# Kernel tuning notes

Hardware: AMD Instinct MI355X
Metric: run time of the kernel (lower is better)

The kernel has to match this reference:

```python
import jax, jax.numpy as jnp
import numpy as np

B, C, H, W = 8, 256, 64, 64
NUM_LABELS = 16  # labels in {-1, 0..15}; -1 means 'no group'


def setup_inputs() -> dict:
    key = jax.random.key(0)
    kx, kl, kw, kb = jax.random.split(key, 4)
    x = jax.random.normal(kx, (B, C, H, W), dtype=jnp.float32)
    # labels in [-1, NUM_LABELS)
    labels = jax.random.randint(kl, (B * C,), 0, NUM_LABELS + 1) - 1
    # groups=C, kernel 1x1: conv weight is (3C,1,1,1) -> per-output-channel scale; bias (3C,)
    w = jax.random.normal(kw, (3 * C,), dtype=jnp.float32) * 0.5
    b = jax.random.normal(kb, (3 * C,), dtype=jnp.float32) * 0.02
    return {"x": x, "labels": labels, "w": w, "b": b}


def reference(x, labels, w, b):
    # x: (B,C,h,w); labels: (B*C,); w,b: (3C,)
    Bv, Cv, hv, wv = x.shape
    hw = hv * wv
    xf = x.reshape(Bv, Cv, hw)
    # grouped 1x1 conv: out channel o (of 3C) reads input channel o//3
    x_rep = jnp.repeat(xf, 3, axis=1)                      # (B,3C,hw)
    qkv = x_rep * w[None, :, None] + b[None, :, None]      # (B,3C,hw)
    flat = qkv.reshape(Bv * 3 * Cv, hw)                    # matches torch reshape(1,3BC,hw)
    BC = Bv * Cv
    q, k, v = flat[:BC], flat[BC:2 * BC], flat[2 * BC:]    # each (BC, hw)
    valid = labels != -1                                   # (BC,)
    same = (labels[:, None] == labels[None, :]) & valid[:, None] & valid[None, :]
    # per-label-group attention == masked dense attention (softmax over same-label cols only)
    scores = q @ k.T                                       # (BC, BC), no sqrt(d) scaling (as in source)
    neg = jnp.finfo(scores.dtype).min
    scores = jnp.where(same, scores, neg)
    weights = jax.nn.softmax(scores, axis=-1)
    out = weights @ v                                      # (BC, hw)
    out = jnp.where(valid[:, None], out, jnp.zeros((), out.dtype))  # -1 rows stay zero
    return out[None]                                       # (1, BC, hw)
```

## Files before the change

### kernel.cpp

```cpp
#include <hip/hip_runtime.h>
#include <cfloat>

#define B_   8
#define C_   256
#define HW_  4096
#define BC_  2048
#define TC_  768
#define NG_  16
#define MAXG 320
#define UK0  682
#define NUQ  683
#define NUK  684
#define NXU  1366
#define NXALL 2048
#define VLO  1280

#define SPLITK 8
#define NT     11
#define NTILES (NT * NT)
#define KSL    (HW_ / SPLITK)
#define WKC    (KSL / 4)
#define NP1    (NUQ * NUK)
#define QMAX   32639

#define MCAP  192
#define CST   192
#define BKP   216

typedef __attribute__((ext_vector_type(8))) short short8;
typedef __attribute__((ext_vector_type(4))) float floatx4;
typedef __attribute__((ext_vector_type(4))) int   intx4;

__device__ __forceinline__ unsigned short f32_to_bf16_rne(float f) {
  unsigned u = __float_as_uint(f);
  unsigned r = (u + 0x7FFFu + ((u >> 16) & 1u)) >> 16;
  return (unsigned short)r;
}

__global__ __launch_bounds__(256) void prep_kernel(
    const float* __restrict__ x, const int* __restrict__ labels,
    char* __restrict__ q8h, char* __restrict__ q8l,
    unsigned short* __restrict__ xhi, float* __restrict__ sums,
    float* __restrict__ scA, float* __restrict__ scB,
    int* __restrict__ grp_n, int* __restrict__ members,
    int* __restrict__ posArr, int nhi)
{
  const int t = threadIdx.x;
  if (blockIdx.x < NG_) {
    __shared__ int lab[BC_];
    __shared__ int cnts[256];
    const int g = blockIdx.x;
    for (int idx = t; idx < BC_; idx += 256) lab[idx] = labels[idx];
    __syncthreads();
    const int base = t * 8;
    int cnt = 0;
#pragma unroll
    for (int k = 0; k < 8; k++) cnt += (lab[base + k] == g) ? 1 : 0;
    cnts[t] = cnt;
    for (int off = 1; off < 256; off <<= 1) {
      __syncthreads();
      const int v = (t >= off) ? cnts[t - off] : 0;
      __syncthreads();
      cnts[t] += v;
    }
    __syncthreads();
    int pos = cnts[t] - cnt;
    if (t == 255) grp_n[g] = cnts[255] < MAXG ? cnts[255] : MAXG;
#pragma unroll
    for (int k = 0; k < 8; k++) {
      const int i = base + k;
      if (lab[i] == g) {
        if (pos < MAXG) { members[g * MAXG + pos] = i; posArr[i] = pos; }
        pos++;
      }
    }
    return;
  }

  const int u = blockIdx.x - NG_;
  if (u >= nhi) return;
  const float* row = x + (size_t)u * HW_;

  if (u < NXU) {
    __shared__ float xs[HW_];
    __shared__ float red[4];
    float s = 0.f, mx = 0.f;
#pragma unroll
    for (int i = 0; i < 4; i++) {
      const int col = i * 1024 + t * 4;
      const float4 v = *(const float4*)(row + col);
      *(float4*)(xs + col) = v;
      s += v.x + v.y + v.z + v.w;
      mx = fmaxf(mx, fmaxf(fmaxf(fabsf(v.x), fabsf(v.y)),
                           fmaxf(fabsf(v.z), fabsf(v.w))));
    }
#pragma unroll
    for (int o = 32; o > 0; o >>= 1) s += __shfl_down(s, o);
    if ((t & 63) == 0) red[t >> 6] = s;
    __syncthreads();
    const float rowsum = red[0] + red[1] + red[2] + red[3];
    __syncthreads();
#pragma unroll
    for (int o = 32; o > 0; o >>= 1) mx = fmaxf(mx, __shfl_down(mx, o));
    if ((t & 63) == 0) red[t >> 6] = mx;
    __syncthreads();
    const float bmax = fmaxf(fmaxf(fmaxf(red[0], red[1]),
                                   fmaxf(red[2], red[3])), 1e-20f);
    if (t == 0) {
      sums[u] = rowsum;
      const float sc = bmax / (float)QMAX;
      if (u < NUQ)  scA[u] = sc;
      if (u >= UK0) scB[u - UK0] = sc;
    }
    const float sinv = (float)QMAX / bmax;
    char* hrow = q8h + (size_t)u * HW_;
    char* lrow = q8l + (size_t)u * HW_;
#pragma unroll
    for (int i = 0; i < 4; i++) {
      const int col = i * 1024 + t * 4;
      char4 hc, lc;
#pragma unroll
      for (int j = 0; j < 4; j++) {
        int q = __float2int_rn(xs[col + j] * sinv);
        q = q > QMAX ? QMAX : (q < -QMAX ? -QMAX : q);
        const int h = (q + 128) >> 8;
        ((char*)&hc)[j] = (char)h;
        ((char*)&lc)[j] = (char)(q - (h << 8));
      }
      *(char4*)(hrow + col) = hc;
      *(char4*)(lrow + col) = lc;
    }
    if (xhi && u >= VLO) {
      unsigned short* hb = xhi + (size_t)u * HW_;
#pragma unroll
      for (int i = 0; i < 4; i++) {
        const int col = i * 1024 + t * 4;
        ushort4 h;
        h.x = f32_to_bf16_rne(xs[col + 0]);
        h.y = f32_to_bf16_rne(xs[col + 1]);
        h.z = f32_to_bf16_rne(xs[col + 2]);
        h.w = f32_to_bf16_rne(xs[col + 3]);
        *(ushort4*)(hb + col) = h;
      }
    }
  } else {
    unsigned short* hb = xhi + (size_t)u * HW_;
#pragma unroll
    for (int i = 0; i < 4; i++) {
      const int col = i * 1024 + t * 4;
      const float4 v = *(const float4*)(row + col);
      ushort4 h;
      h.x = f32_to_bf16_rne(v.x);
      h.y = f32_to_bf16_rne(v.y);
      h.z = f32_to_bf16_rne(v.z);
      h.w = f32_to_bf16_rne(v.w);
      *(ushort4*)(hb + col) = h;
    }
  }
}

__global__ __launch_bounds__(256) void gram_mfma_kernel(
    const char* __restrict__ q8h, const char* __restrict__ q8l,
    float* __restrict__ P,
    const float* __restrict__ w, const float* __restrict__ bbias,
    const float* __restrict__ sums, const int* __restrict__ grp_n,
    const int* __restrict__ members, float4* __restrict__ gtA,
    float2* __restrict__ gtB)
{
  const int bid  = blockIdx.x;
  const int z    = bid & 7;
  const int tile = bid >> 3;
  const int m0 = (tile % NT) * 64;
  const int n0 = (tile / NT) * 64;

  const int t = threadIdx.x;
  const int wave = t >> 6;
  const int lane = t & 63;
  const int fr = lane & 15;
  const int fq = lane >> 4;

  if (z == 0 && tile < NG_) {
    const int g = tile;
    const int n = grp_n[g];
    for (int p = t; p < n; p += 256) {
      const int j = members[g * MAXG + p];
      const int rk = j + BC_;
      const int jk = rk % TC_;
      const int uk = (rk / TC_) * C_ + jk / 3;
      const int jv = (j + 2 * BC_) % TC_;
      gtA[g * MAXG + p] = make_float4(w[jk], bbias[jk], sums[uk], w[jv]);
      gtB[g * MAXG + p] = make_float2(bbias[jv], __int_as_float(uk - UK0));
    }
  }

  const int kbase = z * KSL + wave * WKC + fq * 16;
  const char *pah[4], *pal[4], *pbh[4], *pbl[4];
#pragma unroll
  for (int i = 0; i < 4; i++) {
    const int ar = min(m0 + fr + i * 16, NUQ - 1);
    const int br = min(UK0 + n0 + fr + i * 16, NXU - 1);
    pah[i] = q8h + (size_t)ar * HW_ + kbase;
    pal[i] = q8l + (size_t)ar * HW_ + kbase;
    pbh[i] = q8h + (size_t)br * HW_ + kbase;
    pbl[i] = q8l + (size_t)br * HW_ + kbase;
  }

  intx4 acch[4][4], accx[4][4];
#pragma unroll
  for (int i = 0; i < 4; i++)
#pragma unroll
    for (int j = 0; j < 4; j++) { acch[i][j] = (intx4)(0); accx[i][j] = (intx4)(0); }

  for (int kk = 0; kk < WKC; kk += 64) {
    intx4 ah[4], al[4], bh[4], bl[4];
#pragma unroll
    for (int i = 0; i < 4; i++) {
      ah[i] = *(const intx4*)(pah[i] + kk);
      al[i] = *(const intx4*)(pal[i] + kk);
      bh[i] = *(const intx4*)(pbh[i] + kk);
      bl[i] = *(const intx4*)(pbl[i] + kk);
    }
#pragma unroll
    for (int mt = 0; mt < 4; mt++)
#pragma unroll
      for (int nt = 0; nt < 4; nt++) {
        acch[mt][nt] = __builtin_amdgcn_mfma_i32_16x16x64_i8(ah[mt], bh[nt], acch[mt][nt], 0, 0, 0);
        accx[mt][nt] = __builtin_amdgcn_mfma_i32_16x16x64_i8(ah[mt], bl[nt], accx[mt][nt], 0, 0, 0);
        accx[mt][nt] = __builtin_amdgcn_mfma_i32_16x16x64_i8(al[mt], bh[nt], accx[mt][nt], 0, 0, 0);
      }
  }

  __shared__ float R[2][64][68];
  float* R0 = &R[0][0][0];
  float* R1 = &R[1][0][0];
  if (wave == 0 || wave == 2) {
    float* Rw = (wave == 0) ? R0 : R1;
#pragma unroll
    for (int mt = 0; mt < 4; mt++)
#pragma unroll
      for (int nt = 0; nt < 4; nt++)
#pragma unroll
        for (int r = 0; r < 4; r++)
          Rw[(mt * 16 + fq * 4 + r) * 68 + nt * 16 + fr] =
              65536.f * (float)acch[mt][nt][r] + 256.f * (float)accx[mt][nt][r];
  }
  __syncthreads();
  if (wave == 1 || wave == 3) {
    float* Rw = (wave == 1) ? R0 : R1;
#pragma unroll
    for (int mt = 0; mt < 4; mt++)
#pragma unroll
      for (int nt = 0; nt < 4; nt++)
#pragma unroll
        for (int r = 0; r < 4; r++)
          Rw[(mt * 16 + fq * 4 + r) * 68 + nt * 16 + fr] +=
              65536.f * (float)acch[mt][nt][r] + 256.f * (float)accx[mt][nt][r];
  }
  __syncthreads();
  const int em = t >> 2;
  const int en = (t & 3) * 16;
  const int gm = m0 + em;
  if (gm < NUQ) {
    float* dst = P + (size_t)z * NP1 + (size_t)gm * NUK + n0;
#pragma unroll
    for (int i4 = 0; i4 < 4; i4++) {
      const int n = en + i4 * 4;
      if (n0 + n < NUK) {
        float4 v;
        v.x = R0[em * 68 + n + 0] + R1[em * 68 + n + 0];
        v.y = R0[em * 68 + n + 1] + R1[em * 68 + n + 1];
        v.z = R0[em * 68 + n + 2] + R1[em * 68 + n + 2];
        v.w = R0[em * 68 + n + 3] + R1[em * 68 + n + 3];
        *(float4*)(dst + n) = v;
      }
    }
  }
}

__global__ __launch_bounds__(256) void gram_reduce_kernel(
    const float* __restrict__ P, float* __restrict__ S,
    const float* __restrict__ scA, const float* __restrict__ scB)
{
  const int idx = (blockIdx.x * 256 + threadIdx.x) * 4;
  if (idx < NP1) {
    float4 s = *(const float4*)(P + idx);
#pragma unroll
    for (int sl = 1; sl < SPLITK; sl++) {
      const float4 a = *(const float4*)(P + (size_t)sl * NP1 + idx);
      s.x += a.x; s.y += a.y; s.z += a.z; s.w += a.w;
    }
    const int m = idx / NUK;
    const int n = idx - m * NUK;
    const float sa = scA[m];
    const float4 sb = *(const float4*)(scB + n);
    s.x *= sa * sb.x; s.y *= sa * sb.y; s.z *= sa * sb.z; s.w *= sa * sb.w;
    *(float4*)(S + idx) = s;
  }
}

__device__ __forceinline__ float blockReduceMax(float v, float* red) {
#pragma unroll
  for (int o = 32; o > 0; o >>= 1) v = fmaxf(v, __shfl_down(v, o));
  if ((threadIdx.x & 63) == 0) red[threadIdx.x >> 6] = v;
  __syncthreads();
  v = fmaxf(fmaxf(red[0], red[1]), fmaxf(red[2], red[3]));
  __syncthreads();
  return v;
}
__device__ __forceinline__ float blockReduceSum(float v, float* red) {
#pragma unroll
  for (int o = 32; o > 0; o >>= 1) v += __shfl_down(v, o);
  if ((threadIdx.x & 63) == 0) red[threadIdx.x >> 6] = v;
  __syncthreads();
  v = red[0] + red[1] + red[2] + red[3];
  __syncthreads();
  return v;
}

__global__ __launch_bounds__(256) void softmax_kernel(
    const int* __restrict__ labels, const float* __restrict__ w,
    const float* __restrict__ bbias, const float* __restrict__ sums,
    const float* __restrict__ S, const int* __restrict__ grp_n,
    const int* __restrict__ posArr, const float4* __restrict__ gtA,
    const float2* __restrict__ gtB, unsigned short* __restrict__ coefh,
    float* __restrict__ cb, float* __restrict__ out)
{
  const int i = blockIdx.x;
  const int t = threadIdx.x;
  const int g = labels[i];
  if (g < 0) {
    const float4 z = make_float4(0.f, 0.f, 0.f, 0.f);
    float4* orow = (float4*)(out + (size_t)i * HW_);
    for (int cidx = t; cidx < HW_ / 4; cidx += 256) orow[cidx] = z;
    return;
  }
  __shared__ float red[4];
  const int n   = grp_n[g];
  const int jq  = i % TC_;
  const int uqi = (i / TC_) * C_ + jq / 3;
  const float wq = w[jq], bq = bbias[jq];
  const float sq = sums[uqi];
  const float* Srow = S + (size_t)uqi * NUK;

  const int jj0 = t, jj1 = t + 256;
  float4 A0, A1; float2 B0, B1;
  float s0 = -FLT_MAX, s1 = -FLT_MAX;
  if (jj0 < n) {
    A0 = gtA[g * MAXG + jj0];
    B0 = gtB[g * MAXG + jj0];
    s0 = wq * A0.x * Srow[__float_as_int(B0.y)] + (wq * A0.y) * sq +
         (bq * A0.x) * A0.z + (bq * A0.y) * 4096.f;
  }
  if (jj1 < n) {
    A1 = gtA[g * MAXG + jj1];
    B1 = gtB[g * MAXG + jj1];
    s1 = wq * A1.x * Srow[__float_as_int(B1.y)] + (wq * A1.y) * sq +
         (bq * A1.x) * A1.z + (bq * A1.y) * 4096.f;
  }
  const float mx = blockReduceMax(fmaxf(s0, s1), red);
  const float e0 = (jj0 < n) ? expf(s0 - mx) : 0.f;
  const float e1 = (jj1 < n) ? expf(s1 - mx) : 0.f;
  const float tot = blockReduceSum(e0 + e1, red);
  const float inv = 1.f / tot;

  const int pos = posArr[i];
  unsigned short* crow = coefh + ((size_t)g * MCAP + pos) * CST;
  float lcb = 0.f;
  if (jj0 < n) {
    const float wgt = e0 * inv;
    if (pos < MCAP && jj0 < CST) crow[jj0] = f32_to_bf16_rne(wgt * A0.w);
    lcb += wgt * B0.x;
  } else if (pos < MCAP && jj0 < CST) {
    crow[jj0] = 0;
  }
  if (jj1 < n) {
    const float wgt = e1 * inv;
    lcb += wgt * B1.x;
  }
  const float cbi = blockReduceSum(lcb, red);
  if (t == 0) cb[i] = cbi;
}

__global__ __launch_bounds__(256) void out_mfma_kernel(
    const float* __restrict__ x, const unsigned short* __restrict__ xh,
    const unsigned short* __restrict__ coefh,
    const float* __restrict__ cb, const int* __restrict__ grp_n,
    const int* __restrict__ members, float* __restrict__ out)
{
  const int g  = blockIdx.x;
  const int c0 = blockIdx.y * 64;
  const int n  = min(grp_n[g], MCAP);
  if (n == 0) return;
  const int Kceil = (n + 31) & ~31;
  const int nk8 = Kceil >> 3;
  const int t = threadIdx.x;
  const int wave = t >> 6;
  const int lane = t & 63;
  const int fr = lane & 15;
  const int fq = lane >> 4;

  __shared__ unsigned short Bt[64][BKP];
  __shared__ int   mem[MCAP];
  __shared__ float cbs[MCAP];

  if (t < n) {
    const int j = members[g * MAXG + t];
    mem[t] = j;
    cbs[t] = cb[j];
  }
  __syncthreads();

  {
    const int colq = t & 15;
    const int kcb  = t >> 4;
    for (int kc = kcb; kc < nk8; kc += 16) {
      if (xh) {
        ushort4 hv[8];
#pragma unroll
        for (int j = 0; j < 8; j++) {
          const int k = kc * 8 + j;
          if (k < n) {
            const int jm = mem[k];
            const int rv = jm + 2 * BC_;
            const int uv = (rv / TC_) * C_ + (rv % TC_) / 3;
            hv[j] = *(const ushort4*)(xh + (size_t)uv * HW_ + c0 + colq * 4);
          } else {
            hv[j] = make_ushort4(0, 0, 0, 0);
          }
        }
#pragma unroll
        for (int c = 0; c < 4; c++) {
          short8 pk;
          pk[0] = (short)(c == 0 ? hv[0].x : c == 1 ? hv[0].y : c == 2 ? hv[0].z : hv[0].w);
          pk[1] = (short)(c == 0 ? hv[1].x : c == 1 ? hv[1].y : c == 2 ? hv[1].z : hv[1].w);
          pk[2] = (short)(c == 0 ? hv[2].x : c == 1 ? hv[2].y : c == 2 ? hv[2].z : hv[2].w);
          pk[3] = (short)(c == 0 ? hv[3].x : c == 1 ? hv[3].y : c == 2 ? hv[3].z : hv[3].w);
          pk[4] = (short)(c == 0 ? hv[4].x : c == 1 ? hv[4].y : c == 2 ? hv[4].z : hv[4].w);
          pk[5] = (short)(c == 0 ? hv[5].x : c == 1 ? hv[5].y : c == 2 ? hv[5].z : hv[5].w);
          pk[6] = (short)(c == 0 ? hv[6].x : c == 1 ? hv[6].y : c == 2 ? hv[6].z : hv[6].w);
          pk[7] = (short)(c == 0 ? hv[7].x : c == 1 ? hv[7].y : c == 2 ? hv[7].z : hv[7].w);
          *(short8*)&Bt[colq * 4 + c][kc * 8] = pk;
        }
      } else {
        float4 vals[8];
#pragma unroll
        for (int j = 0; j < 8; j++) {
          const int k = kc * 8 + j;
          if (k < n) {
            const int jm = mem[k];
            const int rv = jm + 2 * BC_;
            const int uv = (rv / TC_) * C_ + (rv % TC_) / 3;
            vals[j] = *(const float4*)(x + (size_t)uv * HW_ + c0 + colq * 4);
          } else {
            vals[j] = make_float4(0.f, 0.f, 0.f, 0.f);
          }
        }
#pragma unroll
        for (int c = 0; c < 4; c++) {
          short8 pk;
          pk[0] = (short)f32_to_bf16_rne(c == 0 ? vals[0].x : c == 1 ? vals[0].y : c == 2 ? vals[0].z : vals[0].w);
          pk[1] = (short)f32_to_bf16_rne(c == 0 ? vals[1].x : c == 1 ? vals[1].y : c == 2 ? vals[1].z : vals[1].w);
          pk[2] = (short)f32_to_bf16_rne(c == 0 ? vals[2].x : c == 1 ? vals[2].y : c == 2 ? vals[2].z : vals[2].w);
          pk[3] = (short)f32_to_bf16_rne(c == 0 ? vals[3].x : c == 1 ? vals[3].y : c == 2 ? vals[3].z : vals[3].w);
          pk[4] = (short)f32_to_bf16_rne(c == 0 ? vals[4].x : c == 1 ? vals[4].y : c == 2 ? vals[4].z : vals[4].w);
          pk[5] = (short)f32_to_bf16_rne(c == 0 ? vals[5].x : c == 1 ? vals[5].y : c == 2 ? vals[5].z : vals[5].w);
          pk[6] = (short)f32_to_bf16_rne(c == 0 ? vals[6].x : c == 1 ? vals[6].y : c == 2 ? vals[6].z : vals[6].w);
          pk[7] = (short)f32_to_bf16_rne(c == 0 ? vals[7].x : c == 1 ? vals[7].y : c == 2 ? vals[7].z : vals[7].w);
          *(short8*)&Bt[colq * 4 + c][kc * 8] = pk;
        }
      }
    }
  }
  __syncthreads();

  const int colw = wave * 16 + fr;

  for (int m0 = 0; m0 < n; m0 += 32) {
    floatx4 acc0 = (floatx4)(0.f), acc1 = (floatx4)(0.f);
    const unsigned short* pa0 = coefh + ((size_t)g * MCAP + m0 + fr) * CST + fq * 8;
    const unsigned short* pa1 = pa0 + 16 * CST;
    for (int k = 0; k < Kceil; k += 32) {
      const short8 a0 = *(const short8*)(pa0 + k);
      const short8 a1 = *(const short8*)(pa1 + k);
      const short8 b  = *(const short8*)&Bt[colw][fq * 8 + k];
      acc0 = __builtin_amdgcn_mfma_f32_16x16x32_bf16(a0, b, acc0, 0, 0, 0);
      acc1 = __builtin_amdgcn_mfma_f32_16x16x32_bf16(a1, b, acc1, 0, 0, 0);
    }
#pragma unroll
    for (int r = 0; r < 4; r++) {
      int m = m0 + fq * 4 + r;
      if (m < n) out[(size_t)mem[m] * HW_ + c0 + colw] = acc0[r] + cbs[m];
      m += 16;
      if (m < n) out[(size_t)mem[m] * HW_ + c0 + colw] = acc1[r] + cbs[m];
    }
  }
}

extern "C" void kernel_launch(void* const* d_in, const int* in_sizes, int n_in,
                              void* d_out, int out_size, void* d_ws, size_t ws_size,
                              hipStream_t stream)
{
  const float* x      = (const float*)d_in[0];
  const int*   labels = (const int*)d_in[1];
  const float* w      = (const float*)d_in[2];
  const float* bb     = (const float*)d_in[3];
  float* out = (float*)d_out;

  char* wsb = (char*)d_ws;
  size_t off = 0;
  auto carve = [&](size_t bytes) -> void* {
    off = (off + 255) & ~(size_t)255;
    void* p = wsb + off;
    off += bytes;
    return p;
  };
  float* sums    = (float*)carve(NXU * sizeof(float));
  float* scA     = (float*)carve(NUQ * sizeof(float));
  float* scB     = (float*)carve(NUK * sizeof(float));
  float* S       = (float*)carve((size_t)NP1 * sizeof(float));
  float* P       = (float*)carve((size_t)SPLITK * NP1 * sizeof(float));
  int*   grp_n   = (int*)carve(NG_ * sizeof(int));
  int*   members = (int*)carve((size_t)NG_ * MAXG * sizeof(int));
  int*   posArr  = (int*)carve(BC_ * sizeof(int));
  unsigned short* coefh = (unsigned short*)carve((size_t)NG_ * MCAP * CST * sizeof(unsigned short));
  float* cb      = (float*)carve(BC_ * sizeof(float));
  float4* gtA    = (float4*)carve((size_t)NG_ * MAXG * sizeof(float4));
  float2* gtB    = (float2*)carve((size_t)NG_ * MAXG * sizeof(float2));
  char*  q8h     = (char*)carve((size_t)NXU * HW_);
  char*  q8l     = (char*)carve((size_t)NXU * HW_);

  const int big = ws_size >= (size_t)47 * 1024 * 1024;
  unsigned short* xhi = big
      ? (unsigned short*)carve((size_t)NXALL * HW_ * sizeof(unsigned short))
      : (unsigned short*)nullptr;
  const int nhi = big ? NXALL : NXU;

  prep_kernel<<<NG_ + nhi, 256, 0, stream>>>(x, labels, q8h, q8l, xhi, sums,
                                             scA, scB, grp_n, members, posArr, nhi);
  gram_mfma_kernel<<<NTILES * SPLITK, 256, 0, stream>>>(
      q8h, q8l, P, w, bb, sums, grp_n, members, gtA, gtB);
  gram_reduce_kernel<<<(NP1 / 4 + 255) / 256, 256, 0, stream>>>(P, S, scA, scB);
  softmax_kernel<<<BC_, 256, 0, stream>>>(labels, w, bb, sums, S, grp_n,
                                          posArr, gtA, gtB, coefh, cb, out);
  out_mfma_kernel<<<dim3(NG_, HW_ / 64), 256, 0, stream>>>(
      x, xhi, coefh, cb, grp_n, members, out);
}
```

Before: 155.5 us.

## Fold split-K gram reduction into softmax and halve split-K factor

Removes the separate gram_reduce kernel: softmax now sums the four split-K partial Gram slices itself, and only at the entries each row gathers. The per-column scale scB is folded into the per-member gather table (now float4). SPLITK drops from 8 to 4, halving the partial buffer and the reduction work, but the gram kernel launches half as many blocks. The workspace threshold for the bf16 x copy is lowered to match the smaller footprint.

```diff
diff --git a/kernel.cpp b/kernel.cpp
--- a/kernel.cpp
+++ b/kernel.cpp
@@ -15,7 +15,7 @@
 #define NXALL 2048
 #define VLO  1280
 
-#define SPLITK 8
+#define SPLITK 4
 #define NT     11
 #define NTILES (NT * NT)
 #define KSL    (HW_ / SPLITK)
@@ -163,13 +163,13 @@
     const char* __restrict__ q8h, const char* __restrict__ q8l,
     float* __restrict__ P,
     const float* __restrict__ w, const float* __restrict__ bbias,
-    const float* __restrict__ sums, const int* __restrict__ grp_n,
-    const int* __restrict__ members, float4* __restrict__ gtA,
-    float2* __restrict__ gtB)
+    const float* __restrict__ sums, const float* __restrict__ scB,
+    const int* __restrict__ grp_n, const int* __restrict__ members,
+    float4* __restrict__ gtA, float4* __restrict__ gtB)
 {
   const int bid  = blockIdx.x;
-  const int z    = bid & 7;
-  const int tile = bid >> 3;
+  const int z    = bid & 3;
+  const int tile = bid >> 2;
   const int m0 = (tile % NT) * 64;
   const int n0 = (tile / NT) * 64;
 
@@ -188,8 +188,10 @@
       const int jk = rk % TC_;
       const int uk = (rk / TC_) * C_ + jk / 3;
       const int jv = (j + 2 * BC_) % TC_;
-      gtA[g * MAXG + p] = make_float4(w[jk], bbias[jk], sums[uk], w[jv]);
-      gtB[g * MAXG + p] = make_float2(bbias[jv], __int_as_float(uk - UK0));
+      const float wk = w[jk];
+      gtA[g * MAXG + p] = make_float4(wk, bbias[jk], sums[uk], w[jv]);
+      gtB[g * MAXG + p] = make_float4(bbias[jv], __int_as_float(uk - UK0),
+                                      wk * scB[uk - UK0], 0.f);
     }
   }
 
@@ -277,27 +279,6 @@
   }
 }
 
-__global__ __launch_bounds__(256) void gram_reduce_kernel(
-    const float* __restrict__ P, float* __restrict__ S,
-    const float* __restrict__ scA, const float* __restrict__ scB)
-{
-  const int idx = (blockIdx.x * 256 + threadIdx.x) * 4;
-  if (idx < NP1) {
-    float4 s = *(const float4*)(P + idx);
-#pragma unroll
-    for (int sl = 1; sl < SPLITK; sl++) {
-      const float4 a = *(const float4*)(P + (size_t)sl * NP1 + idx);
-      s.x += a.x; s.y += a.y; s.z += a.z; s.w += a.w;
-    }
-    const int m = idx / NUK;
-    const int n = idx - m * NUK;
-    const float sa = scA[m];
-    const float4 sb = *(const float4*)(scB + n);
-    s.x *= sa * sb.x; s.y *= sa * sb.y; s.z *= sa * sb.z; s.w *= sa * sb.w;
-    *(float4*)(S + idx) = s;
-  }
-}
-
 __device__ __forceinline__ float blockReduceMax(float v, float* red) {
 #pragma unroll
   for (int o = 32; o > 0; o >>= 1) v = fmaxf(v, __shfl_down(v, o));
@@ -320,10 +301,11 @@
 __global__ __launch_bounds__(256) void softmax_kernel(
     const int* __restrict__ labels, const float* __restrict__ w,
     const float* __restrict__ bbias, const float* __restrict__ sums,
-    const float* __restrict__ S, const int* __restrict__ grp_n,
-    const int* __restrict__ posArr, const float4* __restrict__ gtA,
-    const float2* __restrict__ gtB, unsigned short* __restrict__ coefh,
-    float* __restrict__ cb, float* __restrict__ out)
+    const float* __restrict__ P, const float* __restrict__ scA,
+    const int* __restrict__ grp_n, const int* __restrict__ posArr,
+    const float4* __restrict__ gtA, const float4* __restrict__ gtB,
+    unsigned short* __restrict__ coefh, float* __restrict__ cb,
+    float* __restrict__ out)
 {
   const int i = blockIdx.x;
   const int t = threadIdx.x;
@@ -340,21 +322,28 @@
   const int uqi = (i / TC_) * C_ + jq / 3;
   const float wq = w[jq], bq = bbias[jq];
   const float sq = sums[uqi];
-  const float* Srow = S + (size_t)uqi * NUK;
+  const float wq2 = wq * scA[uqi];
+  const int   pbase = uqi * NUK;
 
   const int jj0 = t, jj1 = t + 256;
-  float4 A0, A1; float2 B0, B1;
+  float4 A0, A1, B0, B1;
   float s0 = -FLT_MAX, s1 = -FLT_MAX;
   if (jj0 < n) {
     A0 = gtA[g * MAXG + jj0];
     B0 = gtB[g * MAXG + jj0];
-    s0 = wq * A0.x * Srow[__float_as_int(B0.y)] + (wq * A0.y) * sq +
+    const int idx = pbase + __float_as_int(B0.y);
+    const float ps = ((P[idx] + P[idx + NP1]) +
+                      (P[idx + 2 * NP1] + P[idx + 3 * NP1]));
+    s0 = wq2 * B0.z * ps + (wq * A0.y) * sq +
          (bq * A0.x) * A0.z + (bq * A0.y) * 4096.f;
   }
   if (jj1 < n) {
     A1 = gtA[g * MAXG + jj1];
     B1 = gtB[g * MAXG + jj1];
-    s1 = wq * A1.x * Srow[__float_as_int(B1.y)] + (wq * A1.y) * sq +
+    const int idx = pbase + __float_as_int(B1.y);
+    const float ps = ((P[idx] + P[idx + NP1]) +
+                      (P[idx + 2 * NP1] + P[idx + 3 * NP1]));
+    s1 = wq2 * B1.z * ps + (wq * A1.y) * sq +
          (bq * A1.x) * A1.z + (bq * A1.y) * 4096.f;
   }
   const float mx = blockReduceMax(fmaxf(s0, s1), red);
@@ -517,7 +506,6 @@
   float* sums    = (float*)carve(NXU * sizeof(float));
   float* scA     = (float*)carve(NUQ * sizeof(float));
   float* scB     = (float*)carve(NUK * sizeof(float));
-  float* S       = (float*)carve((size_t)NP1 * sizeof(float));
   float* P       = (float*)carve((size_t)SPLITK * NP1 * sizeof(float));
   int*   grp_n   = (int*)carve(NG_ * sizeof(int));
   int*   members = (int*)carve((size_t)NG_ * MAXG * sizeof(int));
@@ -525,11 +513,11 @@
   unsigned short* coefh = (unsigned short*)carve((size_t)NG_ * MCAP * CST * sizeof(unsigned short));
   float* cb      = (float*)carve(BC_ * sizeof(float));
   float4* gtA    = (float4*)carve((size_t)NG_ * MAXG * sizeof(float4));
-  float2* gtB    = (float2*)carve((size_t)NG_ * MAXG * sizeof(float2));
+  float4* gtB    = (float4*)carve((size_t)NG_ * MAXG * sizeof(float4));
   char*  q8h     = (char*)carve((size_t)NXU * HW_);
   char*  q8l     = (char*)carve((size_t)NXU * HW_);
 
-  const int big = ws_size >= (size_t)47 * 1024 * 1024;
+  const int big = ws_size >= (size_t)40 * 1024 * 1024;
   unsigned short* xhi = big
       ? (unsigned short*)carve((size_t)NXALL * HW_ * sizeof(unsigned short))
       : (unsigned short*)nullptr;
@@ -538,9 +526,8 @@
   prep_kernel<<<NG_ + nhi, 256, 0, stream>>>(x, labels, q8h, q8l, xhi, sums,
                                              scA, scB, grp_n, members, posArr, nhi);
   gram_mfma_kernel<<<NTILES * SPLITK, 256, 0, stream>>>(
-      q8h, q8l, P, w, bb, sums, grp_n, members, gtA, gtB);
-  gram_reduce_kernel<<<(NP1 / 4 + 255) / 256, 256, 0, stream>>>(P, S, scA, scB);
-  softmax_kernel<<<BC_, 256, 0, stream>>>(labels, w, bb, sums, S, grp_n,
+      q8h, q8l, P, w, bb, sums, scB, grp_n, members, gtA, gtB);
+  softmax_kernel<<<BC_, 256, 0, stream>>>(labels, w, bb, sums, P, scA, grp_n,
                                           posArr, gtA, gtB, coefh, cb, out);
   out_mfma_kernel<<<dim3(NG_, HW_ / 64), 256, 0, stream>>>(
       x, xhi, coefh, cb, grp_n, members, out);
```

Measured after the change: 146.5 us. -5.8%, faster.
